# Kernel optimization log

Measured on AMD Instinct MI355X. Metric: run time of the kernel, lower is better.

## Reference

```python
import jax, jax.numpy as jnp
import numpy as np

B, S, D = 2, 2048, 2048
VOCAB = 32000
CUTOFFS = [1000, 2000, 5000, VOCAB]  # torch appends vocab_size
N_CLUSTERS = 3
HEAD_SIZE = CUTOFFS[0] + N_CLUSTERS  # 1003
LN_EPS = 1e-5
INIT = 0.02


def setup_inputs() -> dict:
    key = jax.random.key(0)
    ks = jax.random.split(key, 10)
    inp = {
        "x": jax.random.normal(ks[0], (B, S, D), dtype=jnp.float32),
        "targets": jax.random.randint(ks[1], (B, S), 0, VOCAB, dtype=jnp.int32),
        "gamma": jnp.ones((D,), jnp.float32),
        "beta": jnp.zeros((D,), jnp.float32),
        "head_w": jax.random.normal(ks[2], (HEAD_SIZE, D), jnp.float32) * INIT,
    }
    # tail clusters: hsz = D // 4**i, osz = cutoffs[i] - cutoffs[i-1]
    for i in range(1, 4):
        hsz = D // (4 ** i)
        osz = CUTOFFS[i] - CUTOFFS[i - 1]
        inp[f"t{i}_w1"] = jax.random.normal(ks[2 + 2 * i], (hsz, D), jnp.float32) * INIT
        inp[f"t{i}_w2"] = jax.random.normal(ks[3 + 2 * i], (osz, hsz), jnp.float32) * INIT
    return inp


def reference(x, targets, gamma, beta, head_w, t1_w1, t1_w2, t2_w1, t2_w2, t3_w1, t3_w2):
    # LayerNorm over last dim
    mu = jnp.mean(x, axis=-1, keepdims=True)
    var = jnp.mean(jnp.square(x - mu), axis=-1, keepdims=True)
    xn = (x - mu) * jax.lax.rsqrt(var + LN_EPS) * gamma + beta

    # shift: predict token t+1 from hidden t
    h = xn[:, :-1, :].reshape(-1, x.shape[-1])      # [N, D]
    lbl = targets[:, 1:].reshape(-1)                # [N]
    n = h.shape[0]
    rows = jnp.arange(n)

    # head: shortlist (first cutoff) + one logit per tail cluster
    head_lp = jax.nn.log_softmax(h @ head_w.T, axis=-1)  # [N, 1003]
    out = head_lp[rows, jnp.clip(lbl, 0, CUTOFFS[0] - 1)]

    tails = [(t1_w1, t1_w2), (t2_w1, t2_w2), (t3_w1, t3_w2)]
    for i, (w1, w2) in enumerate(tails):
        low, high = CUTOFFS[i], CUTOFFS[i + 1]
        tail_lp = jax.nn.log_softmax((h @ w1.T) @ w2.T, axis=-1)  # [N, osz]
        rel = jnp.clip(lbl - low, 0, high - low - 1)
        lp = head_lp[:, CUTOFFS[0] + i] + tail_lp[rows, rel]
        out = jnp.where((lbl >= low) & (lbl < high), lp, out)

    return -jnp.mean(out)  # NLL loss, matches .loss of AdaptiveLogSoftmaxWithLoss
```

## Files before the change

### kernel.cpp

```cpp
#include <hip/hip_runtime.h>
#include <hip/hip_bf16.h>
#include <math.h>

#define BB 2
#define SS 2048
#define DD 2048
#define NR (BB*(SS-1))
#define NRP 4096
#define MT_LD 768
#define MT_P2 512
#define MT_P3 640

#define L2E 1.4426950408889634f
#define LSE_SHIFT 4.0f
#define LSE_NC (-LSE_SHIFT * L2E)
#define WSCALE 16.0f
#define WINV   0.0625f

typedef short  bh8   __attribute__((ext_vector_type(8)));
typedef float  f32x4 __attribute__((ext_vector_type(4)));
typedef long   l64x2 __attribute__((ext_vector_type(2)));

__device__ inline float bfl(unsigned short b) { return __uint_as_float(((unsigned)b) << 16); }
__device__ inline float expsh(float v) { return __builtin_amdgcn_exp2f(fmaf(v, L2E, LSE_NC)); }

__device__ inline float block_sum256(float v) {
    __shared__ float tmp[4];
    #pragma unroll
    for (int o = 32; o > 0; o >>= 1) v += __shfl_down(v, o, 64);
    int lane = threadIdx.x & 63, w = threadIdx.x >> 6;
    if (lane == 0) tmp[w] = v;
    __syncthreads();
    float r = tmp[0] + tmp[1] + tmp[2] + tmp[3];
    __syncthreads();
    return r;
}

__device__ inline unsigned pack_fp8x4(float a, float b, float c, float d) {
    unsigned r = 0;
    r = __builtin_amdgcn_cvt_pk_fp8_f32(a, b, r, false);
    r = __builtin_amdgcn_cvt_pk_fp8_f32(c, d, r, true);
    return r;
}

struct CastSegs {
    const float* src[7];
    void* dst[7];
    int n_src[7];
    int n_tot[7];
    int b0[7];
    int isfp8[7];
};
struct AParams {
    const float* x; const float* gamma; const float* beta;
    unsigned char* h8;
    CastSegs sg; int castBlocks;
    const int* targets;
    int *relH, *rel1, *rel2, *rel3;
    float *S0, *S1, *S2, *out;
};

__global__ __launch_bounds__(256) void stageA(AParams p) {
    int blk = blockIdx.x, tid = threadIdx.x;
    if (blk < NRP) {
        int n = blk;
        unsigned char* hr = p.h8 + (size_t)n * DD;
        if (n >= NR) { *(uint2*)(hr + tid * 8) = make_uint2(0,0); return; }
        int b = n / (SS - 1), t = n % (SS - 1);
        const float4* xr = (const float4*)(p.x + (size_t)(b * SS + t) * DD);
        float4 a = xr[tid * 2];
        float4 c = xr[tid * 2 + 1];
        float sum = a.x + a.y + a.z + a.w + c.x + c.y + c.z + c.w;
        sum = block_sum256(sum);
        float mu = sum * (1.0f / DD);
        float d[8] = {a.x-mu, a.y-mu, a.z-mu, a.w-mu, c.x-mu, c.y-mu, c.z-mu, c.w-mu};
        float sq = 0.f;
        #pragma unroll
        for (int i = 0; i < 8; ++i) sq += d[i] * d[i];
        sq = block_sum256(sq);
        float rstd = rsqrtf(sq * (1.0f / DD) + 1e-5f);
        const float4* g4 = (const float4*)p.gamma;
        const float4* be4 = (const float4*)p.beta;
        float4 g1 = g4[tid*2], g2 = g4[tid*2+1];
        float4 b1 = be4[tid*2], b2 = be4[tid*2+1];
        float gg[8] = {g1.x,g1.y,g1.z,g1.w,g2.x,g2.y,g2.z,g2.w};
        float bb[8] = {b1.x,b1.y,b1.z,b1.w,b2.x,b2.y,b2.z,b2.w};
        float o[8];
        #pragma unroll
        for (int i = 0; i < 8; ++i) o[i] = d[i] * rstd * gg[i] + bb[i];
        uint2 pk;
        pk.x = pack_fp8x4(o[0], o[1], o[2], o[3]);
        pk.y = pack_fp8x4(o[4], o[5], o[6], o[7]);
        *(uint2*)(hr + tid * 8) = pk;
        return;
    }
    blk -= NRP;
    if (blk < p.castBlocks) {
        int k = 0;
        #pragma unroll
        for (int i = 1; i < 7; ++i) if (blk >= p.sg.b0[i]) k = i;
        int i4 = (blk - p.sg.b0[k]) * 1024 + tid * 4;
        if (i4 >= p.sg.n_tot[k]) return;
        float4 v = make_float4(0.f,0.f,0.f,0.f);
        if (i4 < p.sg.n_src[k]) v = *(const float4*)(p.sg.src[k] + i4);
        if (p.sg.isfp8[k]) {
            unsigned pk = pack_fp8x4(v.x * WSCALE, v.y * WSCALE, v.z * WSCALE, v.w * WSCALE);
            *(unsigned*)((unsigned char*)p.sg.dst[k] + i4) = pk;
        } else {
            __align__(8) __hip_bfloat16 o[4] = {
                __float2bfloat16(v.x), __float2bfloat16(v.y),
                __float2bfloat16(v.z), __float2bfloat16(v.w)};
            *(uint2*)((__hip_bfloat16*)p.sg.dst[k] + i4) = *(uint2*)o;
        }
        return;
    }
    blk -= p.castBlocks;
    int n = blk * 256 + tid;
    if (n >= NRP) return;
    int lbl = -1;
    if (n < NR) {
        int b = n / (SS - 1), t = n % (SS - 1);
        lbl = p.targets[b * SS + t + 1];
    }
    bool v = n < NR;
    p.relH[n] = v ? (lbl < 1000 ? lbl : 999) : -1;
    int r1 = lbl - 1000;  p.rel1[n] = v ? (r1 < 0 ? 0 : (r1 > 999   ? 999   : r1)) : -1;
    int r2 = lbl - 2000;  p.rel2[n] = v ? (r2 < 0 ? 0 : (r2 > 2999  ? 2999  : r2)) : -1;
    int r3 = lbl - 5000;  p.rel3[n] = v ? (r3 < 0 ? 0 : (r3 > 26999 ? 26999 : r3)) : -1;
    p.S0[n] = 0.f; p.S1[n] = 0.f; p.S2[n] = 0.f;
    if (n == 0) p.out[0] = 0.f;
}

__global__ __launch_bounds__(256) void megaF(
        const unsigned char* __restrict__ A,
        const unsigned char* __restrict__ W,
        __hip_bfloat16* __restrict__ megaT,
        const int* __restrict__ relH,
        float* __restrict__ S0, float* __restrict__ aux) {
    __shared__ __align__(16) unsigned char As[128 * 64];
    __shared__ __align__(16) unsigned char Ws[128 * 64];
    int tid = threadIdx.x, wv = tid >> 6, lane = tid & 63;
    int row0 = blockIdx.y * 128, col0 = blockIdx.x * 128;
    int wrow = (wv >> 1) * 64, wcol = (wv & 1) * 64;
    f32x4 acc[4][4];
    #pragma unroll
    for (int i = 0; i < 4; ++i)
        #pragma unroll
        for (int j = 0; j < 4; ++j) acc[i][j] = (f32x4){0.f,0.f,0.f,0.f};
    int sr = lane >> 2;
    int kp = (lane & 3) * 16;
    int mrow = lane & 15;
    int q16 = (lane >> 4) * 16;

    for (int k0 = 0; k0 < DD; k0 += 64) {
        __syncthreads();
        #pragma unroll
        for (int i = 0; i < 2; ++i) {
            int chunk = wv * 2 + i;
            int r = chunk * 16 + sr;
            const void* ga = A + (size_t)(row0 + r) * DD + k0 + kp;
            const void* gw = W + (size_t)(col0 + r) * DD + k0 + kp;
            void* la = (char*)As + chunk * 1024 + lane * 16;
            void* lw = (char*)Ws + chunk * 1024 + lane * 16;
            __builtin_amdgcn_global_load_lds(
                (const __attribute__((address_space(1))) void*)ga,
                (__attribute__((address_space(3))) void*)la, 16, 0, 0);
            __builtin_amdgcn_global_load_lds(
                (const __attribute__((address_space(1))) void*)gw,
                (__attribute__((address_space(3))) void*)lw, 16, 0, 0);
        }
        __syncthreads();
        l64x2 af[4], bfr[4];
        #pragma unroll
        for (int t = 0; t < 4; ++t) {
            af[t]  = *(const l64x2*)(As + (wrow + t*16 + mrow) * 64 + q16);
            bfr[t] = *(const l64x2*)(Ws + (wcol + t*16 + mrow) * 64 + q16);
        }
        #pragma unroll
        for (int s = 0; s < 2; ++s)
            #pragma unroll
            for (int i = 0; i < 4; ++i)
                #pragma unroll
                for (int j = 0; j < 4; ++j)
                    acc[i][j] = __builtin_amdgcn_mfma_f32_16x16x32_fp8_fp8(
                        af[i][s], bfr[j][s], acc[i][j], 0, 0, 0);
    }
    int ccol = lane & 15, g = lane >> 4;
    if (blockIdx.x < 8) {
        int grs[4][4], rh[4][4];
        float ps[4][4];
        #pragma unroll
        for (int i = 0; i < 4; ++i)
            #pragma unroll
            for (int r = 0; r < 4; ++r) {
                grs[i][r] = row0 + wrow + i*16 + g*4 + r;
                rh[i][r] = relH[grs[i][r]];
                ps[i][r] = 0.f;
            }
        #pragma unroll
        for (int i = 0; i < 4; ++i)
            #pragma unroll
            for (int j = 0; j < 4; ++j) {
                int gc = col0 + wcol + j*16 + ccol;
                bool inr = gc < 1003;
                #pragma unroll
                for (int r = 0; r < 4; ++r) {
                    float v = acc[i][j][r] * WINV;
                    if (gc == rh[i][r]) aux[grs[i][r]*8 + 0] = v;
                    if (gc >= 1000 && gc < 1003) aux[grs[i][r]*8 + 2 + (gc - 1000)] = v;
                    ps[i][r] += inr ? expsh(v) : 0.f;
                }
            }
        #pragma unroll
        for (int off = 1; off < 16; off <<= 1)
            #pragma unroll
            for (int i = 0; i < 4; ++i)
                #pragma unroll
                for (int r = 0; r < 4; ++r) ps[i][r] += __shfl_xor(ps[i][r], off, 64);
        if (ccol == 0)
            #pragma unroll
            for (int i = 0; i < 4; ++i)
                #pragma unroll
                for (int r = 0; r < 4; ++r) atomicAdd(&S0[grs[i][r]], ps[i][r]);
    } else {
        int cb = col0 - 1024 + wcol;
        #pragma unroll
        for (int i = 0; i < 4; ++i) {
            size_t gr0 = row0 + wrow + i*16 + g*4;
            #pragma unroll
            for (int j = 0; j < 4; ++j) {
                size_t gc = cb + j*16 + ccol;
                #pragma unroll
                for (int r = 0; r < 4; ++r)
                    megaT[(gr0 + r) * MT_LD + gc] = __float2bfloat16(acc[i][j][r] * WINV);
            }
        }
    }
}

__device__ void tail_gemm(const __hip_bfloat16* A, int lda,
        const __hip_bfloat16* W, int K, int bx, int by, int validCols,
        const int* rel, float* S, float* tgt, char* sm) {
    __hip_bfloat16* As = (__hip_bfloat16*)sm;
    __hip_bfloat16* Ws = (__hip_bfloat16*)(sm + 4096);
    int tid = threadIdx.x, wv = tid >> 6, lane = tid & 63;
    int row0 = by * 64, col0 = bx * 128;
    int wrow = (wv >> 1) * 32, wcol = (wv & 1) * 64;
    f32x4 acc[2][4];
    #pragma unroll
    for (int i = 0; i < 2; ++i)
        #pragma unroll
        for (int j = 0; j < 4; ++j) acc[i][j] = (f32x4){0.f,0.f,0.f,0.f};
    int sr = lane >> 2, sk = (lane & 3) * 8, mrow = lane & 15, q16 = (lane >> 4) * 16;

    for (int k0 = 0; k0 < K; k0 += 32) {
        __syncthreads();
        #pragma unroll
        for (int i = 0; i < 3; ++i) {
            int c = wv * 3 + i;
            const __hip_bfloat16* gsrc;
            char* ldst;
            if (c < 4) {
                gsrc = A + (size_t)(row0 + c * 16 + sr) * lda + k0 + sk;
                ldst = (char*)As + c * 1024 + lane * 16;
            } else {
                int cw = c - 4;
                gsrc = W + (size_t)(col0 + cw * 16 + sr) * K + k0 + sk;
                ldst = (char*)Ws + cw * 1024 + lane * 16;
            }
            __builtin_amdgcn_global_load_lds(
                (const __attribute__((address_space(1))) void*)gsrc,
                (__attribute__((address_space(3))) void*)ldst, 16, 0, 0);
        }
        __syncthreads();
        bh8 af[2], bfr[4];
        #pragma unroll
        for (int t = 0; t < 2; ++t)
            af[t] = *(const bh8*)((const char*)As + (wrow + t*16 + mrow) * 64 + q16);
        #pragma unroll
        for (int t = 0; t < 4; ++t)
            bfr[t] = *(const bh8*)((const char*)Ws + (wcol + t*16 + mrow) * 64 + q16);
        #pragma unroll
        for (int i = 0; i < 2; ++i)
            #pragma unroll
            for (int j = 0; j < 4; ++j)
                acc[i][j] = __builtin_amdgcn_mfma_f32_16x16x32_bf16(af[i], bfr[j], acc[i][j], 0, 0, 0);
    }
    int ccol = lane & 15, g = lane >> 4;
    int grs[2][4], rh[2][4];
    float p[2][4];
    #pragma unroll
    for (int i = 0; i < 2; ++i)
        #pragma unroll
        for (int r = 0; r < 4; ++r) {
            grs[i][r] = row0 + wrow + i*16 + g*4 + r;
            rh[i][r] = rel[grs[i][r]];
            p[i][r] = 0.f;
        }
    #pragma unroll
    for (int i = 0; i < 2; ++i)
        #pragma unroll
        for (int j = 0; j < 4; ++j) {
            int gc = col0 + wcol + j*16 + ccol;
            bool inr = gc < validCols;
            #pragma unroll
            for (int r = 0; r < 4; ++r) {
                float v = acc[i][j][r];
                if (gc == rh[i][r]) tgt[grs[i][r]] = v;
                p[i][r] += inr ? expsh(v) : 0.f;
            }
        }
    #pragma unroll
    for (int off = 1; off < 16; off <<= 1)
        #pragma unroll
        for (int i = 0; i < 2; ++i)
            #pragma unroll
            for (int r = 0; r < 4; ++r) p[i][r] += __shfl_xor(p[i][r], off, 64);
    if (ccol == 0)
        #pragma unroll
        for (int i = 0; i < 2; ++i)
            #pragma unroll
            for (int r = 0; r < 4; ++r) atomicAdd(&S[grs[i][r]], p[i][r]);
}

__device__ void t3_partial_body(const __hip_bfloat16* megaT,
        const __hip_bfloat16* w2b, float* pS, int idx, int tid, float* red ) {
    int rg = idx >> 3, cs = idx & 7;
    int wv = tid >> 6, lane = tid & 63;
    int q = lane >> 4, cm = lane & 15;
    int row0 = rg * 64;
    bh8 af[4];
    #pragma unroll
    for (int h = 0; h < 4; ++h)
        af[h] = *(const bh8*)(megaT + (size_t)(row0 + h*16 + cm) * MT_LD + MT_P3 + q * 8);
    int tile0 = cs * 211, tile1 = tile0 + 211;
    float s[4][4];
    #pragma unroll
    for (int h = 0; h < 4; ++h)
        #pragma unroll
        for (int r = 0; r < 4; ++r) s[h][r] = 0.f;
    int ot = tile0 + wv;
    int oc0 = ot < tile1 ? ot : tile1 - 1;
    int oc1 = ot + 4 < tile1 ? ot + 4 : tile1 - 1;
    bh8 b0 = *(const bh8*)(w2b + (size_t)(oc0 * 16 + cm) * 32 + q * 8);
    bh8 b1 = *(const bh8*)(w2b + (size_t)(oc1 * 16 + cm) * 32 + q * 8);
    for (; ot < tile1; ot += 4) {
        bh8 bcur = b0;
        b0 = b1;
        int otn = ot + 8;
        if (otn < tile1)
            b1 = *(const bh8*)(w2b + (size_t)(otn * 16 + cm) * 32 + q * 8);
        f32x4 c[4];
        #pragma unroll
        for (int h = 0; h < 4; ++h)
            c[h] = __builtin_amdgcn_mfma_f32_16x16x32_bf16(af[h], bcur, (f32x4){0,0,0,0}, 0, 0, 0);
        #pragma unroll
        for (int h = 0; h < 4; ++h)
            #pragma unroll
            for (int r = 0; r < 4; ++r) s[h][r] += expsh(c[h][r]);
    }
    #pragma unroll
    for (int off = 1; off < 16; off <<= 1)
        #pragma unroll
        for (int h = 0; h < 4; ++h)
            #pragma unroll
            for (int r = 0; r < 4; ++r) s[h][r] += __shfl_xor(s[h][r], off, 64);
    if (cm == 0)
        #pragma unroll
        for (int h = 0; h < 4; ++h)
            #pragma unroll
            for (int r = 0; r < 4; ++r)
                red[wv * 64 + h*16 + q*4 + r] = s[h][r];
    __syncthreads();
    if (tid < 64)
        pS[(size_t)(row0 + tid) * 8 + cs] = red[tid] + red[64 + tid] + red[128 + tid] + red[192 + tid];
}

__device__ void t3_gather_body(const __hip_bfloat16* megaT, const __hip_bfloat16* w2b,
        const int* rel3, float* tt2, int idx, int tid) {
    int n = idx * 256 + tid;
    if (n >= NR) return;
    int rc = rel3[n];
    const unsigned short* pa = (const unsigned short*)(megaT + (size_t)n * MT_LD + MT_P3);
    const unsigned short* pw = (const unsigned short*)(w2b + (size_t)rc * 32);
    float acc = 0.f;
    #pragma unroll
    for (int k = 0; k < 32; ++k) acc += bfl(pa[k]) * bfl(pw[k]);
    tt2[n] = acc;
}

#define NT3 512
#define NT1 512
#define NT2 1536
__global__ __launch_bounds__(256) void fatC(const __hip_bfloat16* __restrict__ megaT,
        const __hip_bfloat16* __restrict__ t1w2b, const __hip_bfloat16* __restrict__ t2w2b,
        const __hip_bfloat16* __restrict__ w2b3,
        const int* __restrict__ rel1, const int* __restrict__ rel2, const int* __restrict__ rel3,
        float* __restrict__ S1, float* __restrict__ S2, float* __restrict__ pS3,
        float* __restrict__ tt0, float* __restrict__ tt1, float* __restrict__ tt2) {
    __shared__ __align__(16) char sm[12288];
    int idx = blockIdx.x, tid = threadIdx.x;
    if (idx < NT3) { t3_partial_body(megaT, w2b3, pS3, idx, tid, (float*)sm); return; }
    idx -= NT3;
    if (idx < NT1) { tail_gemm(megaT, MT_LD, t1w2b, 512, idx % 8, idx / 8, 1000, rel1, S1, tt0, sm); return; }
    idx -= NT1;
    if (idx < NT2) { tail_gemm(megaT + MT_P2, MT_LD, t2w2b, 128, idx % 24, idx / 24, 3000, rel2, S2, tt1, sm); return; }
    idx -= NT2;
    t3_gather_body(megaT, w2b3, rel3, tt2, idx, tid);
}

__global__ __launch_bounds__(256) void final_kernel(const float* __restrict__ aux,
        const int* __restrict__ targets,
        const float* __restrict__ S0, const float* __restrict__ S1, const float* __restrict__ S2,
        const float* __restrict__ pS3,
        const float* __restrict__ tt0, const float* __restrict__ tt1, const float* __restrict__ tt2,
        float* __restrict__ out) {
    int n = blockIdx.x * 256 + threadIdx.x;
    float local = 0.f;
    if (n < NR) {
        int b = n / (SS - 1), t = n % (SS - 1);
        int lbl = targets[b * SS + t + 1];
        float lse = logf(S0[n]) + LSE_SHIFT;
        float o;
        if (lbl < 1000)      o = aux[n*8 + 0] - lse;
        else if (lbl < 2000) o = (aux[n*8 + 2] - lse) + (tt0[n] - (logf(S1[n]) + LSE_SHIFT));
        else if (lbl < 5000) o = (aux[n*8 + 3] - lse) + (tt1[n] - (logf(S2[n]) + LSE_SHIFT));
        else {
            float S3 = 0.f;
            #pragma unroll
            for (int c = 0; c < 8; ++c) S3 += pS3[n*8 + c];
            S3 -= 8.0f * __builtin_amdgcn_exp2f(LSE_NC);
            o = (aux[n*8 + 4] - lse) + (tt2[n] - (logf(S3) + LSE_SHIFT));
        }
        local = o;
    }
    local = block_sum256(local);
    if (threadIdx.x == 0) atomicAdd(out, -local / (float)NR);
}

extern "C" void kernel_launch(void* const* d_in, const int* in_sizes, int n_in,
                              void* d_out, int out_size, void* d_ws, size_t ws_size,
                              hipStream_t stream) {
    const float* x      = (const float*)d_in[0];
    const int*   targets= (const int*)d_in[1];
    const float* gamma  = (const float*)d_in[2];
    const float* beta   = (const float*)d_in[3];
    const float* head_w = (const float*)d_in[4];
    const float* t1_w1  = (const float*)d_in[5];
    const float* t1_w2  = (const float*)d_in[6];
    const float* t2_w1  = (const float*)d_in[7];
    const float* t2_w2  = (const float*)d_in[8];
    const float* t3_w1  = (const float*)d_in[9];
    const float* t3_w2  = (const float*)d_in[10];
    (void)in_sizes; (void)n_in; (void)out_size; (void)ws_size;

    char* base = (char*)d_ws;
    size_t off = 0;
    auto ab = [&](size_t nbytes) { char* p = base + off; off += (nbytes + 15) & ~(size_t)15; return p; };
    unsigned char* h8     = (unsigned char*)ab((size_t)NRP * DD);
    unsigned char* w1cat8 = (unsigned char*)ab((size_t)1792 * DD);
    __hip_bfloat16* megaT = (__hip_bfloat16*)ab((size_t)NRP * MT_LD * 2);
    __hip_bfloat16* t1w2b = (__hip_bfloat16*)ab((size_t)1024 * 512 * 2);
    __hip_bfloat16* t2w2b = (__hip_bfloat16*)ab((size_t)3072 * 128 * 2);
    __hip_bfloat16* w2b3  = (__hip_bfloat16*)ab((size_t)27008 * 32 * 2);
    float* aux = (float*)ab((size_t)NRP * 8 * 4);
    float* pS3 = (float*)ab((size_t)NRP * 8 * 4);
    float* S0  = (float*)ab(NRP * 4);
    float* S1  = (float*)ab(NRP * 4);
    float* S2  = (float*)ab(NRP * 4);
    int* relH  = (int*)ab(NRP * 4);
    int* rel1  = (int*)ab(NRP * 4);
    int* rel2  = (int*)ab(NRP * 4);
    int* rel3  = (int*)ab(NRP * 4);
    float* tt0 = (float*)ab(NRP * 4);
    float* tt1 = (float*)ab(NRP * 4);
    float* tt2 = (float*)ab(NRP * 4);

    AParams p;
    p.x = x; p.gamma = gamma; p.beta = beta; p.h8 = h8;
    p.targets = targets;
    p.relH = relH; p.rel1 = rel1; p.rel2 = rel2; p.rel3 = rel3;
    p.S0 = S0; p.S1 = S1; p.S2 = S2; p.out = (float*)d_out;
    const float* srcs[7] = {head_w, t1_w1, t2_w1, t3_w1, t1_w2, t2_w2, t3_w2};
    void* dsts[7] = {w1cat8, w1cat8 + (size_t)1024*2048, w1cat8 + (size_t)1536*2048,
                     w1cat8 + (size_t)1664*2048, t1w2b, t2w2b, w2b3};
    int nsrc[7] = {1003*2048, 512*2048, 128*2048, 32*2048, 1000*512, 3000*128, 27000*32};
    int ntot[7] = {1024*2048, 512*2048, 128*2048, 128*2048, 1024*512, 3072*128, 27008*32};
    int isf8[7] = {1, 1, 1, 1, 0, 0, 0};
    int blk = 0;
    for (int i = 0; i < 7; ++i) {
        p.sg.src[i] = srcs[i]; p.sg.dst[i] = dsts[i];
        p.sg.n_src[i] = nsrc[i]; p.sg.n_tot[i] = ntot[i];
        p.sg.isfp8[i] = isf8[i];
        p.sg.b0[i] = blk;
        blk += (ntot[i] + 1023) / 1024;
    }
    p.castBlocks = blk;

    stageA<<<NRP + blk + 16, 256, 0, stream>>>(p);
    megaF<<<dim3(14, 32), 256, 0, stream>>>(h8, w1cat8, megaT, relH, S0, aux);
    fatC<<<NT3 + NT1 + NT2 + 16, 256, 0, stream>>>(megaT, t1w2b, t2w2b, w2b3,
            rel1, rel2, rel3, S1, S2, pS3, tt0, tt1, tt2);
    final_kernel<<<16, 256, 0, stream>>>(aux, targets, S0, S1, S2, pS3, tt0, tt1, tt2, (float*)d_out);
}
```

Before: 187.7 us.

## Double-buffer GEMM LDS staging, split tail-3 wider, fold log2e into weights

Both the fp8 head GEMM and the bf16 tail GEMM now double-buffer their LDS tiles. The next k-slice is prefetched while the current one is computed, with one barrier per iteration instead of two. The tail-3 partial sum-exp work is split 16 ways instead of 8 to raise block count. Its exponent shift is removed by pre-scaling the w2 weights by log2(e), so the kernel uses raw exp2 and the final LSE is corrected in the last kernel. Dropping the shift raises overflow risk if logits grow large, and the change doubles LDS use per block.

```diff
diff --git a/kernel.cpp b/kernel.cpp
--- a/kernel.cpp
+++ b/kernel.cpp
@@ -12,6 +12,7 @@
 #define MT_P3 640
 
 #define L2E 1.4426950408889634f
+#define LN2F 0.6931471805599453f
 #define LSE_SHIFT 4.0f
 #define LSE_NC (-LSE_SHIFT * L2E)
 #define WSCALE 16.0f
@@ -50,6 +51,7 @@
     int n_tot[7];
     int b0[7];
     int isfp8[7];
+    float scl[7];
 };
 struct AParams {
     const float* x; const float* gamma; const float* beta;
@@ -107,9 +109,10 @@
             unsigned pk = pack_fp8x4(v.x * WSCALE, v.y * WSCALE, v.z * WSCALE, v.w * WSCALE);
             *(unsigned*)((unsigned char*)p.sg.dst[k] + i4) = pk;
         } else {
+            float sc = p.sg.scl[k];
             __align__(8) __hip_bfloat16 o[4] = {
-                __float2bfloat16(v.x), __float2bfloat16(v.y),
-                __float2bfloat16(v.z), __float2bfloat16(v.w)};
+                __float2bfloat16(v.x * sc), __float2bfloat16(v.y * sc),
+                __float2bfloat16(v.z * sc), __float2bfloat16(v.w * sc)};
             *(uint2*)((__hip_bfloat16*)p.sg.dst[k] + i4) = *(uint2*)o;
         }
         return;
@@ -137,8 +140,7 @@
         __hip_bfloat16* __restrict__ megaT,
         const int* __restrict__ relH,
         float* __restrict__ S0, float* __restrict__ aux) {
-    __shared__ __align__(16) unsigned char As[128 * 64];
-    __shared__ __align__(16) unsigned char Ws[128 * 64];
+    __shared__ __align__(16) unsigned char smF[2][16384];
     int tid = threadIdx.x, wv = tid >> 6, lane = tid & 63;
     int row0 = blockIdx.y * 128, col0 = blockIdx.x * 128;
     int wrow = (wv >> 1) * 64, wcol = (wv & 1) * 64;
@@ -152,16 +154,15 @@
     int mrow = lane & 15;
     int q16 = (lane >> 4) * 16;
 
-    for (int k0 = 0; k0 < DD; k0 += 64) {
-        __syncthreads();
+    auto stage = [&](int buf, int k0) {
         #pragma unroll
         for (int i = 0; i < 2; ++i) {
             int chunk = wv * 2 + i;
             int r = chunk * 16 + sr;
             const void* ga = A + (size_t)(row0 + r) * DD + k0 + kp;
             const void* gw = W + (size_t)(col0 + r) * DD + k0 + kp;
-            void* la = (char*)As + chunk * 1024 + lane * 16;
-            void* lw = (char*)Ws + chunk * 1024 + lane * 16;
+            void* la = (char*)&smF[buf][0]    + chunk * 1024 + lane * 16;
+            void* lw = (char*)&smF[buf][8192] + chunk * 1024 + lane * 16;
             __builtin_amdgcn_global_load_lds(
                 (const __attribute__((address_space(1))) void*)ga,
                 (__attribute__((address_space(3))) void*)la, 16, 0, 0);
@@ -169,7 +170,17 @@
                 (const __attribute__((address_space(1))) void*)gw,
                 (__attribute__((address_space(3))) void*)lw, 16, 0, 0);
         }
-        __syncthreads();
+    };
+
+    stage(0, 0);
+    asm volatile("s_waitcnt vmcnt(0)" ::: "memory");
+    __builtin_amdgcn_s_barrier();
+    __builtin_amdgcn_sched_barrier(0);
+    int cur = 0;
+    for (int k0 = 0; k0 < DD; k0 += 64) {
+        if (k0 + 64 < DD) stage(cur ^ 1, k0 + 64);
+        const unsigned char* As = &smF[cur][0];
+        const unsigned char* Ws = &smF[cur][8192];
         l64x2 af[4], bfr[4];
         #pragma unroll
         for (int t = 0; t < 4; ++t) {
@@ -184,6 +195,10 @@
                 for (int j = 0; j < 4; ++j)
                     acc[i][j] = __builtin_amdgcn_mfma_f32_16x16x32_fp8_fp8(
                         af[i][s], bfr[j][s], acc[i][j], 0, 0, 0);
+        asm volatile("s_waitcnt vmcnt(0) lgkmcnt(0)" ::: "memory");
+        __builtin_amdgcn_s_barrier();
+        __builtin_amdgcn_sched_barrier(0);
+        cur ^= 1;
     }
     int ccol = lane & 15, g = lane >> 4;
     if (blockIdx.x < 8) {
@@ -241,8 +256,6 @@
 __device__ void tail_gemm(const __hip_bfloat16* A, int lda,
         const __hip_bfloat16* W, int K, int bx, int by, int validCols,
         const int* rel, float* S, float* tgt, char* sm) {
-    __hip_bfloat16* As = (__hip_bfloat16*)sm;
-    __hip_bfloat16* Ws = (__hip_bfloat16*)(sm + 4096);
     int tid = threadIdx.x, wv = tid >> 6, lane = tid & 63;
     int row0 = by * 64, col0 = bx * 128;
     int wrow = (wv >> 1) * 32, wcol = (wv & 1) * 64;
@@ -252,9 +265,10 @@
         #pragma unroll
         for (int j = 0; j < 4; ++j) acc[i][j] = (f32x4){0.f,0.f,0.f,0.f};
     int sr = lane >> 2, sk = (lane & 3) * 8, mrow = lane & 15, q16 = (lane >> 4) * 16;
-
-    for (int k0 = 0; k0 < K; k0 += 32) {
-        __syncthreads();
+    int nt = K >> 5;
+
+    auto stage = [&](int buf, int k0) {
+        char* base = sm + buf * 12288;
         #pragma unroll
         for (int i = 0; i < 3; ++i) {
             int c = wv * 3 + i;
@@ -262,29 +276,43 @@
             char* ldst;
             if (c < 4) {
                 gsrc = A + (size_t)(row0 + c * 16 + sr) * lda + k0 + sk;
-                ldst = (char*)As + c * 1024 + lane * 16;
+                ldst = base + c * 1024 + lane * 16;
             } else {
                 int cw = c - 4;
                 gsrc = W + (size_t)(col0 + cw * 16 + sr) * K + k0 + sk;
-                ldst = (char*)Ws + cw * 1024 + lane * 16;
+                ldst = base + 4096 + cw * 1024 + lane * 16;
             }
             __builtin_amdgcn_global_load_lds(
                 (const __attribute__((address_space(1))) void*)gsrc,
                 (__attribute__((address_space(3))) void*)ldst, 16, 0, 0);
         }
-        __syncthreads();
+    };
+
+    stage(0, 0);
+    asm volatile("s_waitcnt vmcnt(0)" ::: "memory");
+    __builtin_amdgcn_s_barrier();
+    __builtin_amdgcn_sched_barrier(0);
+    int cur = 0;
+    for (int t = 0; t < nt; ++t) {
+        if (t + 1 < nt) stage(cur ^ 1, (t + 1) << 5);
+        const char* As = sm + cur * 12288;
+        const char* Ws = As + 4096;
         bh8 af[2], bfr[4];
         #pragma unroll
-        for (int t = 0; t < 2; ++t)
-            af[t] = *(const bh8*)((const char*)As + (wrow + t*16 + mrow) * 64 + q16);
-        #pragma unroll
-        for (int t = 0; t < 4; ++t)
-            bfr[t] = *(const bh8*)((const char*)Ws + (wcol + t*16 + mrow) * 64 + q16);
+        for (int u = 0; u < 2; ++u)
+            af[u] = *(const bh8*)(As + (wrow + u*16 + mrow) * 64 + q16);
+        #pragma unroll
+        for (int u = 0; u < 4; ++u)
+            bfr[u] = *(const bh8*)(Ws + (wcol + u*16 + mrow) * 64 + q16);
         #pragma unroll
         for (int i = 0; i < 2; ++i)
             #pragma unroll
             for (int j = 0; j < 4; ++j)
                 acc[i][j] = __builtin_amdgcn_mfma_f32_16x16x32_bf16(af[i], bfr[j], acc[i][j], 0, 0, 0);
+        asm volatile("s_waitcnt vmcnt(0) lgkmcnt(0)" ::: "memory");
+        __builtin_amdgcn_s_barrier();
+        __builtin_amdgcn_sched_barrier(0);
+        cur ^= 1;
     }
     int ccol = lane & 15, g = lane >> 4;
     int grs[2][4], rh[2][4];
@@ -323,9 +351,12 @@
             for (int r = 0; r < 4; ++r) atomicAdd(&S[grs[i][r]], p[i][r]);
 }
 
+#define T3_TILES 1688
+#define T3_SPLIT 16
+#define T3_TPC   106
 __device__ void t3_partial_body(const __hip_bfloat16* megaT,
         const __hip_bfloat16* w2b, float* pS, int idx, int tid, float* red ) {
-    int rg = idx >> 3, cs = idx & 7;
+    int rg = idx >> 4, cs = idx & 15;
     int wv = tid >> 6, lane = tid & 63;
     int q = lane >> 4, cm = lane & 15;
     int row0 = rg * 64;
@@ -333,7 +364,8 @@
     #pragma unroll
     for (int h = 0; h < 4; ++h)
         af[h] = *(const bh8*)(megaT + (size_t)(row0 + h*16 + cm) * MT_LD + MT_P3 + q * 8);
-    int tile0 = cs * 211, tile1 = tile0 + 211;
+    int tile0 = cs * T3_TPC;
+    int tile1 = tile0 + T3_TPC; if (tile1 > T3_TILES) tile1 = T3_TILES;
     float s[4][4];
     #pragma unroll
     for (int h = 0; h < 4; ++h)
@@ -357,7 +389,7 @@
         #pragma unroll
         for (int h = 0; h < 4; ++h)
             #pragma unroll
-            for (int r = 0; r < 4; ++r) s[h][r] += expsh(c[h][r]);
+            for (int r = 0; r < 4; ++r) s[h][r] += __builtin_amdgcn_exp2f(c[h][r]);
     }
     #pragma unroll
     for (int off = 1; off < 16; off <<= 1)
@@ -373,7 +405,7 @@
                 red[wv * 64 + h*16 + q*4 + r] = s[h][r];
     __syncthreads();
     if (tid < 64)
-        pS[(size_t)(row0 + tid) * 8 + cs] = red[tid] + red[64 + tid] + red[128 + tid] + red[192 + tid];
+        pS[(size_t)(row0 + tid) * 16 + cs] = red[tid] + red[64 + tid] + red[128 + tid] + red[192 + tid];
 }
 
 __device__ void t3_gather_body(const __hip_bfloat16* megaT, const __hip_bfloat16* w2b,
@@ -389,7 +421,7 @@
     tt2[n] = acc;
 }
 
-#define NT3 512
+#define NT3 1024
 #define NT1 512
 #define NT2 1536
 __global__ __launch_bounds__(256) void fatC(const __hip_bfloat16* __restrict__ megaT,
@@ -398,7 +430,7 @@
         const int* __restrict__ rel1, const int* __restrict__ rel2, const int* __restrict__ rel3,
         float* __restrict__ S1, float* __restrict__ S2, float* __restrict__ pS3,
         float* __restrict__ tt0, float* __restrict__ tt1, float* __restrict__ tt2) {
-    __shared__ __align__(16) char sm[12288];
+    __shared__ __align__(16) char sm[24576];
     int idx = blockIdx.x, tid = threadIdx.x;
     if (idx < NT3) { t3_partial_body(megaT, w2b3, pS3, idx, tid, (float*)sm); return; }
     idx -= NT3;
@@ -428,9 +460,9 @@
         else {
             float S3 = 0.f;
             #pragma unroll
-            for (int c = 0; c < 8; ++c) S3 += pS3[n*8 + c];
-            S3 -= 8.0f * __builtin_amdgcn_exp2f(LSE_NC);
-            o = (aux[n*8 + 4] - lse) + (tt2[n] - (logf(S3) + LSE_SHIFT));
+            for (int c = 0; c < 16; ++c) S3 += pS3[n*16 + c];
+            S3 -= 8.0f;
+            o = (aux[n*8 + 4] - lse) + (tt2[n] * LN2F - logf(S3));
         }
         local = o;
     }
@@ -464,7 +496,7 @@
     __hip_bfloat16* t2w2b = (__hip_bfloat16*)ab((size_t)3072 * 128 * 2);
     __hip_bfloat16* w2b3  = (__hip_bfloat16*)ab((size_t)27008 * 32 * 2);
     float* aux = (float*)ab((size_t)NRP * 8 * 4);
-    float* pS3 = (float*)ab((size_t)NRP * 8 * 4);
+    float* pS3 = (float*)ab((size_t)NRP * 16 * 4);
     float* S0  = (float*)ab(NRP * 4);
     float* S1  = (float*)ab(NRP * 4);
     float* S2  = (float*)ab(NRP * 4);
@@ -487,11 +519,13 @@
     int nsrc[7] = {1003*2048, 512*2048, 128*2048, 32*2048, 1000*512, 3000*128, 27000*32};
     int ntot[7] = {1024*2048, 512*2048, 128*2048, 128*2048, 1024*512, 3072*128, 27008*32};
     int isf8[7] = {1, 1, 1, 1, 0, 0, 0};
+    float scls[7] = {1.f, 1.f, 1.f, 1.f, 1.0f, 1.0f, L2E};
     int blk = 0;
     for (int i = 0; i < 7; ++i) {
         p.sg.src[i] = srcs[i]; p.sg.dst[i] = dsts[i];
         p.sg.n_src[i] = nsrc[i]; p.sg.n_tot[i] = ntot[i];
         p.sg.isfp8[i] = isf8[i];
+        p.sg.scl[i] = scls[i];
         p.sg.b0[i] = blk;
         blk += (ntot[i] + 1023) / 1024;
     }
```

Result: no change. 190.9 us (+1.7%).
